# Optimization experiments

Measured on AMD Instinct MI355X. Metric: run time of the kernel, lower is better.

Reference implementation:

```python
import jax, jax.numpy as jnp
import numpy as np

B, F, V, E, D1, DD, L2 = 4096, 32, 50000, 64, 256, 16, 128


def setup_inputs() -> dict:
    key = jax.random.key(0)
    ks = jax.random.split(key, 16)
    s = 0.05  # small init scale to keep tanh unsaturated
    return {
        "sparse": jax.random.randint(ks[0], (B, F), 0, V, dtype=jnp.int32),
        "dense": jax.random.normal(ks[1], (B, DD), dtype=jnp.float32),
        "tables": jax.random.normal(ks[2], (F, V, E), dtype=jnp.float32) * s,
        "Wz": jax.random.normal(ks[3], (D1, F, E), dtype=jnp.float32) * s,
        "bz": jnp.zeros((D1,), jnp.float32),
        "Wpi": jax.random.normal(ks[4], (D1, F, F), dtype=jnp.float32) * s,
        "bpi": jnp.zeros((D1,), jnp.float32),
        "Wpo": jax.random.normal(ks[5], (D1, E, E), dtype=jnp.float32) * s,
        "bpo": jnp.zeros((D1,), jnp.float32),
        "B1": jax.random.normal(ks[6], (D1,), dtype=jnp.float32) * s,
        "W1": jax.random.normal(ks[7], (D1 + DD, D1), dtype=jnp.float32) * s,
        "b1": jnp.zeros((D1,), jnp.float32),
        "W2": jax.random.normal(ks[8], (D1, L2), dtype=jnp.float32) * s,
        "b2": jnp.zeros((L2,), jnp.float32),
        "W3": jax.random.normal(ks[9], (L2, 1), dtype=jnp.float32) * s,
        "b3": jnp.zeros((1,), jnp.float32),
    }


def reference(sparse, dense, tables, Wz, bz, Wpi, bpi, Wpo, bpo, B1,
              W1, b1, W2, b2, W3, b3):
    # Embedding lookup: per-field table gather -> [B, F, E]
    emb = tables[jnp.arange(F)[None, :], sparse]
    # Lz: Conv1d(in=F, kernel=E) over [B, F, E] == full contraction -> [B, D1]
    Lz = jnp.einsum('bfe,dfe->bd', emb, Wz) + bz
    # Inner product: [B, F, F], then Conv1d(in=F, kernel=F) full contraction
    inner = jnp.einsum('bie,bje->bij', emb, emb)
    Lp_inner = jnp.einsum('bij,dij->bd', inner, Wpi) + bpi
    # Outer product: sum_{i,j} x_i^T x_j == s^T s with s = sum_i x_i (exact rewrite)
    s = emb.sum(axis=1)                      # [B, E]
    outer = s[:, :, None] * s[:, None, :]    # [B, E, E]
    Lp_outer = jnp.einsum('bij,dij->bd', outer, Wpo) + bpo
    L1 = Lz + Lp_inner + Lp_outer + B1       # [B, D1]
    deep_x = jnp.concatenate([L1, dense], axis=1)  # [B, D1+DD]
    h = jnp.tanh(deep_x @ W1 + b1)
    h = jnp.tanh(h @ W2 + b2)
    out = (h @ W3 + b3)[:, 0]                # [B]
    return out
```

## Files before the change

### kernel.cpp

```cpp
#include <hip/hip_runtime.h>
#include <hip/hip_bf16.h>

#define B_    4096
#define F_    32
#define V_    50000
#define E_    64
#define D1_   256
#define DD_   16
#define L2N_  128
#define KX    3072
#define KTOT  7168
#define NKC   8

typedef __bf16 bf16x8 __attribute__((ext_vector_type(8)));
typedef float  f32x4  __attribute__((ext_vector_type(4)));

typedef __attribute__((address_space(1))) const void gvoid;
typedef __attribute__((address_space(3))) void svoid;

__device__ __forceinline__ ushort f2b(float f){
  __bf16 h = (__bf16)f; return __builtin_bit_cast(ushort, h);
}
__device__ __forceinline__ float b2f(ushort u){
  return __uint_as_float(((uint)u) << 16);
}
__device__ __forceinline__ float blo(uint u){ return __uint_as_float(u << 16); }
__device__ __forceinline__ float bhi(uint u){ return __uint_as_float(u & 0xffff0000u); }
__device__ __forceinline__ void gload16(const void* g, void* l){
  __builtin_amdgcn_global_load_lds((gvoid*)g, (svoid*)l, 16, 0, 0);
}

__global__ __launch_bounds__(256) void prep_gather(
    const float* __restrict__ Wz, const float* __restrict__ Wpi,
    const float* __restrict__ Wpo, const float* __restrict__ W1,
    const float* __restrict__ W2,
    const int* __restrict__ sparse, const float* __restrict__ tables,
    ushort* __restrict__ WBb, ushort* __restrict__ W1b, ushort* __restrict__ W2b,
    ushort* __restrict__ Xb, ushort* __restrict__ Sb) {
  __shared__ ushort gsh[4][32 * 72];
  int bid = blockIdx.x, t = threadIdx.x;
  if (bid < 640) {
    if (bid < 256) {
      int n = bid;
#pragma unroll
      for (int j = 0; j < 7; ++j) {
        int k4 = (j * 256 + t) * 4;
        float4 v;
        if (k4 < 2048)      v = *(const float4*)&Wz [(size_t)n * 2048 + k4];
        else if (k4 < 3072) v = *(const float4*)&Wpi[(size_t)n * 1024 + (k4 - 2048)];
        else                v = *(const float4*)&Wpo[(size_t)n * 4096 + (k4 - 3072)];
        ushort4 o = make_ushort4(f2b(v.x), f2b(v.y), f2b(v.z), f2b(v.w));
        *(ushort4*)&WBb[(size_t)n * KTOT + k4] = o;
      }
    } else if (bid < 512) {
      int n = bid - 256;
      float v0 = (t < 272) ? W1[(size_t)t * 256 + n] : 0.f;
      W1b[(size_t)n * 288 + t] = f2b(v0);
      if (t < 32) {
        int k2 = 256 + t;
        float v1 = (k2 < 272) ? W1[(size_t)k2 * 256 + n] : 0.f;
        W1b[(size_t)n * 288 + k2] = f2b(v1);
      }
    } else {
      int n = bid - 512;
      W2b[(size_t)n * 256 + t] = f2b(W2[(size_t)t * 128 + n]);
    }
    return;
  }

  int w = t >> 6, l = t & 63;
  int b = (bid - 640) * 4 + w;
  int fr = l & 15, q = l >> 4;

  int i0 = sparse[b * F_ + fr];
  int i1 = sparse[b * F_ + 16 + fr];
  const float* r0 = tables + ((size_t)fr * V_ + i0) * 64;
  const float* r1 = tables + ((size_t)(16 + fr) * V_ + i1) * 64;

  float4 v[2][2][2];
#pragma unroll
  for (int ks = 0; ks < 2; ++ks) {
    v[0][ks][0] = *(const float4*)(r0 + ks * 32 + q * 8);
    v[0][ks][1] = *(const float4*)(r0 + ks * 32 + q * 8 + 4);
    v[1][ks][0] = *(const float4*)(r1 + ks * 32 + q * 8);
    v[1][ks][1] = *(const float4*)(r1 + ks * 32 + q * 8 + 4);
  }

  bf16x8 fg[2][2];
#pragma unroll
  for (int rh = 0; rh < 2; ++rh)
#pragma unroll
    for (int ks = 0; ks < 2; ++ks) {
      bf16x8 a;
      a[0] = (__bf16)v[rh][ks][0].x; a[1] = (__bf16)v[rh][ks][0].y;
      a[2] = (__bf16)v[rh][ks][0].z; a[3] = (__bf16)v[rh][ks][0].w;
      a[4] = (__bf16)v[rh][ks][1].x; a[5] = (__bf16)v[rh][ks][1].y;
      a[6] = (__bf16)v[rh][ks][1].z; a[7] = (__bf16)v[rh][ks][1].w;
      fg[rh][ks] = a;
      *(bf16x8*)&Xb[(size_t)b * KX + (rh * 16 + fr) * 64 + ks * 32 + q * 8] = a;
    }

  float sv[2][8];
#pragma unroll
  for (int ks = 0; ks < 2; ++ks) {
    sv[ks][0] = v[0][ks][0].x + v[1][ks][0].x; sv[ks][1] = v[0][ks][0].y + v[1][ks][0].y;
    sv[ks][2] = v[0][ks][0].z + v[1][ks][0].z; sv[ks][3] = v[0][ks][0].w + v[1][ks][0].w;
    sv[ks][4] = v[0][ks][1].x + v[1][ks][1].x; sv[ks][5] = v[0][ks][1].y + v[1][ks][1].y;
    sv[ks][6] = v[0][ks][1].z + v[1][ks][1].z; sv[ks][7] = v[0][ks][1].w + v[1][ks][1].w;
  }
#pragma unroll
  for (int m = 1; m < 16; m <<= 1)
#pragma unroll
    for (int ks = 0; ks < 2; ++ks)
#pragma unroll
      for (int j = 0; j < 8; ++j)
        sv[ks][j] += __shfl_xor(sv[ks][j], m, 64);
  if (fr == 0) {
#pragma unroll
    for (int ks = 0; ks < 2; ++ks) {
      ushort4 o0 = make_ushort4(f2b(sv[ks][0]), f2b(sv[ks][1]), f2b(sv[ks][2]), f2b(sv[ks][3]));
      ushort4 o1 = make_ushort4(f2b(sv[ks][4]), f2b(sv[ks][5]), f2b(sv[ks][6]), f2b(sv[ks][7]));
      *(ushort4*)&Sb[(size_t)b * 64 + ks * 32 + q * 8]     = o0;
      *(ushort4*)&Sb[(size_t)b * 64 + ks * 32 + q * 8 + 4] = o1;
    }
  }

  f32x4 g[2][2] = {};
#pragma unroll
  for (int ks = 0; ks < 2; ++ks)
#pragma unroll
    for (int ri = 0; ri < 2; ++ri)
#pragma unroll
      for (int rj = 0; rj < 2; ++rj)
        g[ri][rj] = __builtin_amdgcn_mfma_f32_16x16x32_bf16(
            fg[ri][ks], fg[rj][ks], g[ri][rj], 0, 0, 0);

#pragma unroll
  for (int ri = 0; ri < 2; ++ri)
#pragma unroll
    for (int rj = 0; rj < 2; ++rj)
#pragma unroll
      for (int r = 0; r < 4; ++r)
        gsh[w][(ri * 16 + q * 4 + r) * 72 + rj * 16 + fr] = f2b(g[ri][rj][r]);
  {
    int rrow = l >> 1, rcol = (l & 1) * 16;
    uint4 ga = *(const uint4*)&gsh[w][rrow * 72 + rcol];
    uint4 gb = *(const uint4*)&gsh[w][rrow * 72 + rcol + 8];
    size_t dst = (size_t)b * KX + 2048 + rrow * 32 + rcol;
    *(uint4*)&Xb[dst]     = ga;
    *(uint4*)&Xb[dst + 8] = gb;
  }
}

__global__ __launch_bounds__(512, 1) void gemm_l1(
    const ushort* __restrict__ Xb, const ushort* __restrict__ WBb,
    const ushort* __restrict__ Sb, ushort* __restrict__ Lp) {
  __shared__ __align__(16) ushort As[2][128 * 64];
  __shared__ __align__(16) ushort Bs[2][256 * 64];
  __shared__ ushort Ssl[128 * 18];

  int bid = blockIdx.x;
  int kc  = bid & 7;
  int mT  = bid >> 3;
  int bRow = mT * 128;
  int kt0 = kc * 14;
  int i_start = min(max(0, kt0 - 48), 48);

  int tid = threadIdx.x, w = tid >> 6, l = tid & 63;
  int wm = (w >> 2) * 64, wn = (w & 3) * 64;
  int fr = l & 15, q = l >> 4;

#pragma unroll
  for (int r = 0; r < 2; ++r) {
    int p = r * 1024 + tid * 2;
    int row = p >> 4, col = p & 15;
    *(ushort2*)&Ssl[row * 18 + col] =
        *(const ushort2*)&Sb[(size_t)(bRow + row) * 64 + i_start + col];
  }

  uint4 sregu[4][2];
#pragma unroll
  for (int mi = 0; mi < 4; ++mi) {
    int grow = bRow + wm + mi * 16 + fr;
    sregu[mi][0] = *(const uint4*)&Sb[(size_t)grow * 64 + q * 8];
    sregu[mi][1] = *(const uint4*)&Sb[(size_t)grow * 64 + 32 + q * 8];
  }

  int r8 = l >> 3;
  int sg = ((l & 7) ^ r8) * 8;

  auto stageA = [&](int bI, int kt) {
    const ushort* src = Xb + (size_t)(bRow + w * 16 + r8) * KX + kt * 64 + sg;
#pragma unroll
    for (int c = 0; c < 2; ++c)
      gload16(src + (size_t)(c * 8) * KX, &As[bI][(w * 16 + c * 8) * 64]);
  };
  auto stageB = [&](int bI, int kt) {
    const ushort* src = WBb + (size_t)(w * 32 + r8) * KTOT + kt * 64 + sg;
#pragma unroll
    for (int c = 0; c < 4; ++c)
      gload16(src + (size_t)(c * 8) * KTOT, &Bs[bI][(w * 32 + c * 8) * 64]);
  };

  f32x4 acc[4][4] = {};
  bf16x8 af[4][2], bfr[4][2];
  int buf = 0;

  if (kt0 < 48) stageA(0, kt0);
  stageB(0, kt0);
  __syncthreads();

#pragma unroll
  for (int tl = 0; tl < 14; ++tl) {
    int kt = kt0 + tl;
    if (tl + 1 < 14) {
      if (kt + 1 < 48) stageA(buf ^ 1, kt + 1);
      stageB(buf ^ 1, kt + 1);
    }

#pragma unroll
    for (int ni = 0; ni < 4; ++ni) {
      int col = wn + ni * 16 + fr;
#pragma unroll
      for (int ks = 0; ks < 2; ++ks) {
        int slot = (ks * 4 + q) ^ (col & 7);
        bfr[ni][ks] = *(const bf16x8*)&Bs[buf][col * 64 + slot * 8];
      }
    }
    if (kt < 48) {
#pragma unroll
      for (int mi = 0; mi < 4; ++mi) {
        int row = wm + mi * 16 + fr;
#pragma unroll
        for (int ks = 0; ks < 2; ++ks) {
          int slot = (ks * 4 + q) ^ (row & 7);
          af[mi][ks] = *(const bf16x8*)&As[buf][row * 64 + slot * 8];
        }
      }
    } else {
      int iloc = kt - 48 - i_start;
#pragma unroll
      for (int mi = 0; mi < 4; ++mi) {
        float si = b2f(Ssl[(wm + mi * 16 + fr) * 18 + iloc]);
#pragma unroll
        for (int ks = 0; ks < 2; ++ks) {
          uint4 uv = sregu[mi][ks];
          bf16x8 a;
          a[0] = (__bf16)(si * blo(uv.x)); a[1] = (__bf16)(si * bhi(uv.x));
          a[2] = (__bf16)(si * blo(uv.y)); a[3] = (__bf16)(si * bhi(uv.y));
          a[4] = (__bf16)(si * blo(uv.z)); a[5] = (__bf16)(si * bhi(uv.z));
          a[6] = (__bf16)(si * blo(uv.w)); a[7] = (__bf16)(si * bhi(uv.w));
          af[mi][ks] = a;
        }
      }
    }
#pragma unroll
    for (int ks = 0; ks < 2; ++ks)
#pragma unroll
      for (int mi = 0; mi < 4; ++mi)
#pragma unroll
        for (int ni = 0; ni < 4; ++ni)
          acc[mi][ni] = __builtin_amdgcn_mfma_f32_16x16x32_bf16(
              af[mi][ks], bfr[ni][ks], acc[mi][ni], 0, 0, 0);
    __syncthreads();
    buf ^= 1;
  }

  ushort* Lpk = Lp + (size_t)kc * (B_ * D1_);
#pragma unroll
  for (int mi = 0; mi < 4; ++mi) {
    int row0 = bRow + wm + mi * 16 + q * 4;
#pragma unroll
    for (int ni = 0; ni < 4; ++ni) {
      int col = wn + ni * 16 + fr;
#pragma unroll
      for (int r = 0; r < 4; ++r)
        Lpk[(size_t)(row0 + r) * D1_ + col] = f2b(acc[mi][ni][r]);
    }
  }
}

__global__ __launch_bounds__(256) void mlp_fused(
    const ushort* __restrict__ Lp, const float* __restrict__ dense,
    const ushort* __restrict__ W1b, const ushort* __restrict__ W2b,
    const float* __restrict__ bz, const float* __restrict__ bpi,
    const float* __restrict__ bpo, const float* __restrict__ B1v,
    const float* __restrict__ b1, const float* __restrict__ b2,
    const float* __restrict__ W3, const float* __restrict__ b3,
    float* __restrict__ out) {
  __shared__ ushort hs[16 * 264];
  __shared__ ushort h2s[16 * 136];
  __shared__ float bvs[256];
  int b0 = blockIdx.x * 16;
  int tid = threadIdx.x, w = tid >> 6, l = tid & 63;
  int row = l & 15, q = l >> 4;
  int wn = w * 64;

  bvs[tid] = bz[tid] + bpi[tid] + bpo[tid] + B1v[tid];
  __syncthreads();

  f32x4 acc1[4] = {};
  for (int kt = 0; kt < 9; ++kt) {
    int k0 = kt * 32 + q * 8;
    bf16x8 afr;
    if (kt < 8) {
      size_t base = (size_t)(b0 + row) * D1_ + k0;
      float s[8] = {0.f, 0.f, 0.f, 0.f, 0.f, 0.f, 0.f, 0.f};
#pragma unroll
      for (int p = 0; p < NKC; ++p) {
        uint4 u = *(const uint4*)&Lp[(size_t)p * (B_ * D1_) + base];
        s[0] += blo(u.x); s[1] += bhi(u.x);
        s[2] += blo(u.y); s[3] += bhi(u.y);
        s[4] += blo(u.z); s[5] += bhi(u.z);
        s[6] += blo(u.w); s[7] += bhi(u.w);
      }
      float4 bv0 = *(const float4*)&bvs[k0];
      float4 bv1 = *(const float4*)&bvs[k0 + 4];
      afr[0] = (__bf16)(s[0] + bv0.x); afr[1] = (__bf16)(s[1] + bv0.y);
      afr[2] = (__bf16)(s[2] + bv0.z); afr[3] = (__bf16)(s[3] + bv0.w);
      afr[4] = (__bf16)(s[4] + bv1.x); afr[5] = (__bf16)(s[5] + bv1.y);
      afr[6] = (__bf16)(s[6] + bv1.z); afr[7] = (__bf16)(s[7] + bv1.w);
    } else if (q < 2) {
      float4 u0 = *(const float4*)&dense[(size_t)(b0 + row) * DD_ + q * 8];
      float4 u1 = *(const float4*)&dense[(size_t)(b0 + row) * DD_ + q * 8 + 4];
      afr[0] = (__bf16)u0.x; afr[1] = (__bf16)u0.y; afr[2] = (__bf16)u0.z; afr[3] = (__bf16)u0.w;
      afr[4] = (__bf16)u1.x; afr[5] = (__bf16)u1.y; afr[6] = (__bf16)u1.z; afr[7] = (__bf16)u1.w;
    } else {
      afr = (bf16x8)(__bf16)0.f;
    }
#pragma unroll
    for (int ni = 0; ni < 4; ++ni) {
      bf16x8 bfr = *(const bf16x8*)&W1b[(size_t)(wn + ni * 16 + row) * 288 + k0];
      acc1[ni] = __builtin_amdgcn_mfma_f32_16x16x32_bf16(afr, bfr, acc1[ni], 0, 0, 0);
    }
  }
#pragma unroll
  for (int ni = 0; ni < 4; ++ni) {
    int col = wn + ni * 16 + row;
    float bias = b1[col];
#pragma unroll
    for (int r = 0; r < 4; ++r)
      hs[(q * 4 + r) * 264 + col] = f2b(tanhf(acc1[ni][r] + bias));
  }
  __syncthreads();

  int wn2 = w * 32;
  f32x4 acc2[2] = {};
  for (int kt = 0; kt < 8; ++kt) {
    int k0 = kt * 32 + q * 8;
    bf16x8 afr = *(const bf16x8*)&hs[row * 264 + k0];
#pragma unroll
    for (int ni = 0; ni < 2; ++ni) {
      bf16x8 bfr = *(const bf16x8*)&W2b[(size_t)(wn2 + ni * 16 + row) * 256 + k0];
      acc2[ni] = __builtin_amdgcn_mfma_f32_16x16x32_bf16(afr, bfr, acc2[ni], 0, 0, 0);
    }
  }
#pragma unroll
  for (int ni = 0; ni < 2; ++ni) {
    int col = wn2 + ni * 16 + row;
    float bias = b2[col];
#pragma unroll
    for (int r = 0; r < 4; ++r)
      h2s[(q * 4 + r) * 136 + col] = f2b(tanhf(acc2[ni][r] + bias));
  }
  __syncthreads();

  if (w == 0) {
    int rr = l >> 2, g = l & 3;
    float sum = 0.f;
#pragma unroll
    for (int jj = 0; jj < 32; ++jj) {
      int j = g * 32 + jj;
      sum += b2f(h2s[rr * 136 + j]) * W3[j];
    }
    sum += __shfl_xor(sum, 1, 64);
    sum += __shfl_xor(sum, 2, 64);
    if (g == 0) out[b0 + rr] = sum + b3[0];
  }
}

extern "C" void kernel_launch(void* const* d_in, const int* in_sizes, int n_in,
                              void* d_out, int out_size, void* d_ws, size_t ws_size,
                              hipStream_t stream) {
  const int*   sparse = (const int*)  d_in[0];
  const float* dense  = (const float*)d_in[1];
  const float* tables = (const float*)d_in[2];
  const float* Wz     = (const float*)d_in[3];
  const float* bz     = (const float*)d_in[4];
  const float* Wpi    = (const float*)d_in[5];
  const float* bpi    = (const float*)d_in[6];
  const float* Wpo    = (const float*)d_in[7];
  const float* bpo    = (const float*)d_in[8];
  const float* B1v    = (const float*)d_in[9];
  const float* W1     = (const float*)d_in[10];
  const float* b1     = (const float*)d_in[11];
  const float* W2     = (const float*)d_in[12];
  const float* b2     = (const float*)d_in[13];
  const float* W3     = (const float*)d_in[14];
  const float* b3     = (const float*)d_in[15];
  float* out = (float*)d_out;

  char* ws = (char*)d_ws;
  ushort* Xb  = (ushort*)(ws);
  ushort* WBb = (ushort*)(ws + 25165824);
  ushort* W1b = (ushort*)(ws + 28835840);
  ushort* W2b = (ushort*)(ws + 28983296);
  ushort* Sb  = (ushort*)(ws + 29048832);
  ushort* Lp  = (ushort*)(ws + 29573120);

  prep_gather<<<dim3(1664), dim3(256), 0, stream>>>(
      Wz, Wpi, Wpo, W1, W2, sparse, tables, WBb, W1b, W2b, Xb, Sb);
  gemm_l1    <<<dim3(256),  dim3(512), 0, stream>>>(Xb, WBb, Sb, Lp);
  mlp_fused  <<<dim3(256),  dim3(256), 0, stream>>>(
      Lp, dense, W1b, W2b, bz, bpi, bpo, B1v, b1, b2, W3, b3, out);
}
```

Measured before the change: 59.77 us.

## Fuse L1 GEMM and MLP into one launch with per-tile atomic counters

Merges the split-K L1 GEMM and the MLP kernels into a single 384-block launch. The extra 128 blocks spin on a per-row-tile atomic counter until all eight K-chunks for their 128 rows are written, then run the MLP on 32 rows each. The counters are reset in the prep kernel. This removes one kernel launch boundary and lets the MLP start early for finished tiles. In exchange it relies on forward progress of the waiting blocks (deadlock risk if consumer blocks occupy CUs before producers), and the MLP blocks now use 512 threads and the large shared allocation.

Result: slower. 153.5 us (+156.9%).

```diff
diff --git a/kernel.cpp b/kernel.cpp
--- a/kernel.cpp
+++ b/kernel.cpp
@@ -36,10 +36,11 @@
     const float* __restrict__ W2,
     const int* __restrict__ sparse, const float* __restrict__ tables,
     ushort* __restrict__ WBb, ushort* __restrict__ W1b, ushort* __restrict__ W2b,
-    ushort* __restrict__ Xb, ushort* __restrict__ Sb) {
+    ushort* __restrict__ Xb, ushort* __restrict__ Sb, int* __restrict__ cnt) {
   __shared__ ushort gsh[4][32 * 72];
   int bid = blockIdx.x, t = threadIdx.x;
   if (bid < 640) {
+    if (bid == 0 && t < 32) cnt[t] = 0;
     if (bid < 256) {
       int n = bid;
 #pragma unroll
@@ -152,230 +153,258 @@
   }
 }
 
-__global__ __launch_bounds__(512, 1) void gemm_l1(
+__global__ __launch_bounds__(512, 1) void gemm_mlp(
     const ushort* __restrict__ Xb, const ushort* __restrict__ WBb,
-    const ushort* __restrict__ Sb, ushort* __restrict__ Lp) {
-  __shared__ __align__(16) ushort As[2][128 * 64];
-  __shared__ __align__(16) ushort Bs[2][256 * 64];
-  __shared__ ushort Ssl[128 * 18];
-
-  int bid = blockIdx.x;
-  int kc  = bid & 7;
-  int mT  = bid >> 3;
-  int bRow = mT * 128;
-  int kt0 = kc * 14;
-  int i_start = min(max(0, kt0 - 48), 48);
-
-  int tid = threadIdx.x, w = tid >> 6, l = tid & 63;
-  int wm = (w >> 2) * 64, wn = (w & 3) * 64;
-  int fr = l & 15, q = l >> 4;
-
-#pragma unroll
-  for (int r = 0; r < 2; ++r) {
-    int p = r * 1024 + tid * 2;
-    int row = p >> 4, col = p & 15;
-    *(ushort2*)&Ssl[row * 18 + col] =
-        *(const ushort2*)&Sb[(size_t)(bRow + row) * 64 + i_start + col];
-  }
-
-  uint4 sregu[4][2];
-#pragma unroll
-  for (int mi = 0; mi < 4; ++mi) {
-    int grow = bRow + wm + mi * 16 + fr;
-    sregu[mi][0] = *(const uint4*)&Sb[(size_t)grow * 64 + q * 8];
-    sregu[mi][1] = *(const uint4*)&Sb[(size_t)grow * 64 + 32 + q * 8];
-  }
-
-  int r8 = l >> 3;
-  int sg = ((l & 7) ^ r8) * 8;
-
-  auto stageA = [&](int bI, int kt) {
-    const ushort* src = Xb + (size_t)(bRow + w * 16 + r8) * KX + kt * 64 + sg;
-#pragma unroll
-    for (int c = 0; c < 2; ++c)
-      gload16(src + (size_t)(c * 8) * KX, &As[bI][(w * 16 + c * 8) * 64]);
-  };
-  auto stageB = [&](int bI, int kt) {
-    const ushort* src = WBb + (size_t)(w * 32 + r8) * KTOT + kt * 64 + sg;
-#pragma unroll
-    for (int c = 0; c < 4; ++c)
-      gload16(src + (size_t)(c * 8) * KTOT, &Bs[bI][(w * 32 + c * 8) * 64]);
-  };
-
-  f32x4 acc[4][4] = {};
-  bf16x8 af[4][2], bfr[4][2];
-  int buf = 0;
-
-  if (kt0 < 48) stageA(0, kt0);
-  stageB(0, kt0);
-  __syncthreads();
-
-#pragma unroll
-  for (int tl = 0; tl < 14; ++tl) {
-    int kt = kt0 + tl;
-    if (tl + 1 < 14) {
-      if (kt + 1 < 48) stageA(buf ^ 1, kt + 1);
-      stageB(buf ^ 1, kt + 1);
-    }
-
-#pragma unroll
-    for (int ni = 0; ni < 4; ++ni) {
-      int col = wn + ni * 16 + fr;
-#pragma unroll
-      for (int ks = 0; ks < 2; ++ks) {
-        int slot = (ks * 4 + q) ^ (col & 7);
-        bfr[ni][ks] = *(const bf16x8*)&Bs[buf][col * 64 + slot * 8];
-      }
-    }
-    if (kt < 48) {
-#pragma unroll
-      for (int mi = 0; mi < 4; ++mi) {
-        int row = wm + mi * 16 + fr;
-#pragma unroll
-        for (int ks = 0; ks < 2; ++ks) {
-          int slot = (ks * 4 + q) ^ (row & 7);
-          af[mi][ks] = *(const bf16x8*)&As[buf][row * 64 + slot * 8];
-        }
-      }
-    } else {
-      int iloc = kt - 48 - i_start;
-#pragma unroll
-      for (int mi = 0; mi < 4; ++mi) {
-        float si = b2f(Ssl[(wm + mi * 16 + fr) * 18 + iloc]);
-#pragma unroll
-        for (int ks = 0; ks < 2; ++ks) {
-          uint4 uv = sregu[mi][ks];
-          bf16x8 a;
-          a[0] = (__bf16)(si * blo(uv.x)); a[1] = (__bf16)(si * bhi(uv.x));
-          a[2] = (__bf16)(si * blo(uv.y)); a[3] = (__bf16)(si * bhi(uv.y));
-          a[4] = (__bf16)(si * blo(uv.z)); a[5] = (__bf16)(si * bhi(uv.z));
-          a[6] = (__bf16)(si * blo(uv.w)); a[7] = (__bf16)(si * bhi(uv.w));
-          af[mi][ks] = a;
-        }
-      }
-    }
-#pragma unroll
-    for (int ks = 0; ks < 2; ++ks)
-#pragma unroll
-      for (int mi = 0; mi < 4; ++mi)
-#pragma unroll
-        for (int ni = 0; ni < 4; ++ni)
-          acc[mi][ni] = __builtin_amdgcn_mfma_f32_16x16x32_bf16(
-              af[mi][ks], bfr[ni][ks], acc[mi][ni], 0, 0, 0);
-    __syncthreads();
-    buf ^= 1;
-  }
-
-  ushort* Lpk = Lp + (size_t)kc * (B_ * D1_);
-#pragma unroll
-  for (int mi = 0; mi < 4; ++mi) {
-    int row0 = bRow + wm + mi * 16 + q * 4;
-#pragma unroll
-    for (int ni = 0; ni < 4; ++ni) {
-      int col = wn + ni * 16 + fr;
-#pragma unroll
-      for (int r = 0; r < 4; ++r)
-        Lpk[(size_t)(row0 + r) * D1_ + col] = f2b(acc[mi][ni][r]);
-    }
-  }
-}
-
-__global__ __launch_bounds__(256) void mlp_fused(
-    const ushort* __restrict__ Lp, const float* __restrict__ dense,
+    const ushort* __restrict__ Sb, ushort* __restrict__ Lp,
+    const float* __restrict__ dense,
     const ushort* __restrict__ W1b, const ushort* __restrict__ W2b,
     const float* __restrict__ bz, const float* __restrict__ bpi,
     const float* __restrict__ bpo, const float* __restrict__ B1v,
     const float* __restrict__ b1, const float* __restrict__ b2,
     const float* __restrict__ W3, const float* __restrict__ b3,
-    float* __restrict__ out) {
-  __shared__ ushort hs[16 * 264];
-  __shared__ ushort h2s[16 * 136];
-  __shared__ float bvs[256];
-  int b0 = blockIdx.x * 16;
+    int* __restrict__ cnt, float* __restrict__ out) {
+  __shared__ __align__(16) ushort smem[51456];
+
+  int bid = blockIdx.x;
   int tid = threadIdx.x, w = tid >> 6, l = tid & 63;
-  int row = l & 15, q = l >> 4;
-  int wn = w * 64;
-
-  bvs[tid] = bz[tid] + bpi[tid] + bpo[tid] + B1v[tid];
-  __syncthreads();
-
-  f32x4 acc1[4] = {};
-  for (int kt = 0; kt < 9; ++kt) {
-    int k0 = kt * 32 + q * 8;
-    bf16x8 afr;
-    if (kt < 8) {
-      size_t base = (size_t)(b0 + row) * D1_ + k0;
-      float s[8] = {0.f, 0.f, 0.f, 0.f, 0.f, 0.f, 0.f, 0.f};
-#pragma unroll
-      for (int p = 0; p < NKC; ++p) {
-        uint4 u = *(const uint4*)&Lp[(size_t)p * (B_ * D1_) + base];
-        s[0] += blo(u.x); s[1] += bhi(u.x);
-        s[2] += blo(u.y); s[3] += bhi(u.y);
-        s[4] += blo(u.z); s[5] += bhi(u.z);
-        s[6] += blo(u.w); s[7] += bhi(u.w);
-      }
-      float4 bv0 = *(const float4*)&bvs[k0];
-      float4 bv1 = *(const float4*)&bvs[k0 + 4];
-      afr[0] = (__bf16)(s[0] + bv0.x); afr[1] = (__bf16)(s[1] + bv0.y);
-      afr[2] = (__bf16)(s[2] + bv0.z); afr[3] = (__bf16)(s[3] + bv0.w);
-      afr[4] = (__bf16)(s[4] + bv1.x); afr[5] = (__bf16)(s[5] + bv1.y);
-      afr[6] = (__bf16)(s[6] + bv1.z); afr[7] = (__bf16)(s[7] + bv1.w);
-    } else if (q < 2) {
-      float4 u0 = *(const float4*)&dense[(size_t)(b0 + row) * DD_ + q * 8];
-      float4 u1 = *(const float4*)&dense[(size_t)(b0 + row) * DD_ + q * 8 + 4];
-      afr[0] = (__bf16)u0.x; afr[1] = (__bf16)u0.y; afr[2] = (__bf16)u0.z; afr[3] = (__bf16)u0.w;
-      afr[4] = (__bf16)u1.x; afr[5] = (__bf16)u1.y; afr[6] = (__bf16)u1.z; afr[7] = (__bf16)u1.w;
-    } else {
-      afr = (bf16x8)(__bf16)0.f;
+  int fr = l & 15, q = l >> 4;
+
+  if (bid < 256) {
+    ushort* As0 = smem;
+    ushort* As1 = As0 + 128 * 64;
+    ushort* Bs0 = As1 + 128 * 64;
+    ushort* Bs1 = Bs0 + 256 * 64;
+    ushort* Ssl = Bs1 + 256 * 64;
+
+    int kc  = bid & 7;
+    int mT  = bid >> 3;
+    int bRow = mT * 128;
+    int kt0 = kc * 14;
+    int i_start = min(max(0, kt0 - 48), 48);
+
+    int wm = (w >> 2) * 64, wn = (w & 3) * 64;
+
+#pragma unroll
+    for (int r = 0; r < 2; ++r) {
+      int p = r * 1024 + tid * 2;
+      int row = p >> 4, col = p & 15;
+      *(ushort2*)&Ssl[row * 18 + col] =
+          *(const ushort2*)&Sb[(size_t)(bRow + row) * 64 + i_start + col];
+    }
+
+    uint4 sregu[4][2];
+#pragma unroll
+    for (int mi = 0; mi < 4; ++mi) {
+      int grow = bRow + wm + mi * 16 + fr;
+      sregu[mi][0] = *(const uint4*)&Sb[(size_t)grow * 64 + q * 8];
+      sregu[mi][1] = *(const uint4*)&Sb[(size_t)grow * 64 + 32 + q * 8];
+    }
+
+    int r8 = l >> 3;
+    int sg = ((l & 7) ^ r8) * 8;
+
+    auto stageA = [&](ushort* dst, int kt) {
+      const ushort* src = Xb + (size_t)(bRow + w * 16 + r8) * KX + kt * 64 + sg;
+#pragma unroll
+      for (int c = 0; c < 2; ++c)
+        gload16(src + (size_t)(c * 8) * KX, &dst[(w * 16 + c * 8) * 64]);
+    };
+    auto stageB = [&](ushort* dst, int kt) {
+      const ushort* src = WBb + (size_t)(w * 32 + r8) * KTOT + kt * 64 + sg;
+#pragma unroll
+      for (int c = 0; c < 4; ++c)
+        gload16(src + (size_t)(c * 8) * KTOT, &dst[(w * 32 + c * 8) * 64]);
+    };
+
+    f32x4 acc[4][4] = {};
+    bf16x8 af[4][2], bfr[4][2];
+
+    if (kt0 < 48) stageA(As0, kt0);
+    stageB(Bs0, kt0);
+    __syncthreads();
+
+#pragma unroll
+    for (int tl = 0; tl < 14; ++tl) {
+      int kt = kt0 + tl;
+      ushort* Ac = (tl & 1) ? As1 : As0;
+      ushort* Bc = (tl & 1) ? Bs1 : Bs0;
+      ushort* An = (tl & 1) ? As0 : As1;
+      ushort* Bn = (tl & 1) ? Bs0 : Bs1;
+      if (tl + 1 < 14) {
+        if (kt + 1 < 48) stageA(An, kt + 1);
+        stageB(Bn, kt + 1);
+      }
+
+#pragma unroll
+      for (int ni = 0; ni < 4; ++ni) {
+        int col = wn + ni * 16 + fr;
+#pragma unroll
+        for (int ks = 0; ks < 2; ++ks) {
+          int slot = (ks * 4 + q) ^ (col & 7);
+          bfr[ni][ks] = *(const bf16x8*)&Bc[col * 64 + slot * 8];
+        }
+      }
+      if (kt < 48) {
+#pragma unroll
+        for (int mi = 0; mi < 4; ++mi) {
+          int row = wm + mi * 16 + fr;
+#pragma unroll
+          for (int ks = 0; ks < 2; ++ks) {
+            int slot = (ks * 4 + q) ^ (row & 7);
+            af[mi][ks] = *(const bf16x8*)&Ac[row * 64 + slot * 8];
+          }
+        }
+      } else {
+        int iloc = kt - 48 - i_start;
+#pragma unroll
+        for (int mi = 0; mi < 4; ++mi) {
+          float si = b2f(Ssl[(wm + mi * 16 + fr) * 18 + iloc]);
+#pragma unroll
+          for (int ks = 0; ks < 2; ++ks) {
+            uint4 uv = sregu[mi][ks];
+            bf16x8 a;
+            a[0] = (__bf16)(si * blo(uv.x)); a[1] = (__bf16)(si * bhi(uv.x));
+            a[2] = (__bf16)(si * blo(uv.y)); a[3] = (__bf16)(si * bhi(uv.y));
+            a[4] = (__bf16)(si * blo(uv.z)); a[5] = (__bf16)(si * bhi(uv.z));
+            a[6] = (__bf16)(si * blo(uv.w)); a[7] = (__bf16)(si * bhi(uv.w));
+            af[mi][ks] = a;
+          }
+        }
+      }
+#pragma unroll
+      for (int ks = 0; ks < 2; ++ks)
+#pragma unroll
+        for (int mi = 0; mi < 4; ++mi)
+#pragma unroll
+          for (int ni = 0; ni < 4; ++ni)
+            acc[mi][ni] = __builtin_amdgcn_mfma_f32_16x16x32_bf16(
+                af[mi][ks], bfr[ni][ks], acc[mi][ni], 0, 0, 0);
+      __syncthreads();
+    }
+
+    ushort* Lpk = Lp + (size_t)kc * (B_ * D1_);
+#pragma unroll
+    for (int mi = 0; mi < 4; ++mi) {
+      int row0 = bRow + wm + mi * 16 + q * 4;
+#pragma unroll
+      for (int ni = 0; ni < 4; ++ni) {
+        int col = wn + ni * 16 + fr;
+#pragma unroll
+        for (int r = 0; r < 4; ++r)
+          Lpk[(size_t)(row0 + r) * D1_ + col] = f2b(acc[mi][ni][r]);
+      }
+    }
+
+    __threadfence();
+    __syncthreads();
+    if (tid == 0) atomicAdd(&cnt[mT], 1);
+    return;
+  }
+
+  {
+    int bid2 = bid - 256;
+    int b0   = bid2 * 32;
+    int mT   = bid2 >> 2;
+
+    if (tid == 0) {
+      while (__hip_atomic_load(&cnt[mT], __ATOMIC_RELAXED,
+                               __HIP_MEMORY_SCOPE_AGENT) < NKC)
+        __builtin_amdgcn_s_sleep(8);
+    }
+    __syncthreads();
+    __threadfence();
+
+    ushort* hs  = smem;
+    ushort* h2s = smem + 32 * 264;
+    float*  bvs = (float*)(smem + 32 * 264 + 32 * 136);
+
+    if (tid < 256) bvs[tid] = bz[tid] + bpi[tid] + bpo[tid] + B1v[tid];
+    __syncthreads();
+
+    int rg = w >> 2;
+    int cg = w & 3;
+    int row = fr;
+    int rr = rg * 16;
+
+    int wn1 = cg * 64;
+    f32x4 acc1[4] = {};
+    for (int kt = 0; kt < 9; ++kt) {
+      int k0 = kt * 32 + q * 8;
+      bf16x8 afr;
+      if (kt < 8) {
+        size_t base = (size_t)(b0 + rr + row) * D1_ + k0;
+        float s[8] = {0.f, 0.f, 0.f, 0.f, 0.f, 0.f, 0.f, 0.f};
+#pragma unroll
+        for (int p = 0; p < NKC; ++p) {
+          uint4 u = *(const uint4*)&Lp[(size_t)p * (B_ * D1_) + base];
+          s[0] += blo(u.x); s[1] += bhi(u.x);
+          s[2] += blo(u.y); s[3] += bhi(u.y);
+          s[4] += blo(u.z); s[5] += bhi(u.z);
+          s[6] += blo(u.w); s[7] += bhi(u.w);
+        }
+        float4 bv0 = *(const float4*)&bvs[k0];
+        float4 bv1 = *(const float4*)&bvs[k0 + 4];
+        afr[0] = (__bf16)(s[0] + bv0.x); afr[1] = (__bf16)(s[1] + bv0.y);
+        afr[2] = (__bf16)(s[2] + bv0.z); afr[3] = (__bf16)(s[3] + bv0.w);
+        afr[4] = (__bf16)(s[4] + bv1.x); afr[5] = (__bf16)(s[5] + bv1.y);
+        afr[6] = (__bf16)(s[6] + bv1.z); afr[7] = (__bf16)(s[7] + bv1.w);
+      } else if (q < 2) {
+        float4 u0 = *(const float4*)&dense[(size_t)(b0 + rr + row) * DD_ + q * 8];
+        float4 u1 = *(const float4*)&dense[(size_t)(b0 + rr + row) * DD_ + q * 8 + 4];
+        afr[0] = (__bf16)u0.x; afr[1] = (__bf16)u0.y; afr[2] = (__bf16)u0.z; afr[3] = (__bf16)u0.w;
+        afr[4] = (__bf16)u1.x; afr[5] = (__bf16)u1.y; afr[6] = (__bf16)u1.z; afr[7] = (__bf16)u1.w;
+      } else {
+        afr = (bf16x8)(__bf16)0.f;
+      }
+#pragma unroll
+      for (int ni = 0; ni < 4; ++ni) {
+        bf16x8 bfr = *(const bf16x8*)&W1b[(size_t)(wn1 + ni * 16 + row) * 288 + k0];
+        acc1[ni] = __builtin_amdgcn_mfma_f32_16x16x32_bf16(afr, bfr, acc1[ni], 0, 0, 0);
+      }
     }
 #pragma unroll
     for (int ni = 0; ni < 4; ++ni) {
-      bf16x8 bfr = *(const bf16x8*)&W1b[(size_t)(wn + ni * 16 + row) * 288 + k0];
-      acc1[ni] = __builtin_amdgcn_mfma_f32_16x16x32_bf16(afr, bfr, acc1[ni], 0, 0, 0);
-    }
-  }
-#pragma unroll
-  for (int ni = 0; ni < 4; ++ni) {
-    int col = wn + ni * 16 + row;
-    float bias = b1[col];
-#pragma unroll
-    for (int r = 0; r < 4; ++r)
-      hs[(q * 4 + r) * 264 + col] = f2b(tanhf(acc1[ni][r] + bias));
-  }
-  __syncthreads();
-
-  int wn2 = w * 32;
-  f32x4 acc2[2] = {};
-  for (int kt = 0; kt < 8; ++kt) {
-    int k0 = kt * 32 + q * 8;
-    bf16x8 afr = *(const bf16x8*)&hs[row * 264 + k0];
+      int col = wn1 + ni * 16 + row;
+      float bias = b1[col];
+#pragma unroll
+      for (int r = 0; r < 4; ++r)
+        hs[(rr + q * 4 + r) * 264 + col] = f2b(tanhf(acc1[ni][r] + bias));
+    }
+    __syncthreads();
+
+    int wn2 = cg * 32;
+    f32x4 acc2[2] = {};
+    for (int kt = 0; kt < 8; ++kt) {
+      int k0 = kt * 32 + q * 8;
+      bf16x8 afr = *(const bf16x8*)&hs[(rr + row) * 264 + k0];
+#pragma unroll
+      for (int ni = 0; ni < 2; ++ni) {
+        bf16x8 bfr = *(const bf16x8*)&W2b[(size_t)(wn2 + ni * 16 + row) * 256 + k0];
+        acc2[ni] = __builtin_amdgcn_mfma_f32_16x16x32_bf16(afr, bfr, acc2[ni], 0, 0, 0);
+      }
+    }
 #pragma unroll
     for (int ni = 0; ni < 2; ++ni) {
-      bf16x8 bfr = *(const bf16x8*)&W2b[(size_t)(wn2 + ni * 16 + row) * 256 + k0];
-      acc2[ni] = __builtin_amdgcn_mfma_f32_16x16x32_bf16(afr, bfr, acc2[ni], 0, 0, 0);
-    }
-  }
-#pragma unroll
-  for (int ni = 0; ni < 2; ++ni) {
-    int col = wn2 + ni * 16 + row;
-    float bias = b2[col];
-#pragma unroll
-    for (int r = 0; r < 4; ++r)
-      h2s[(q * 4 + r) * 136 + col] = f2b(tanhf(acc2[ni][r] + bias));
-  }
-  __syncthreads();
-
-  if (w == 0) {
-    int rr = l >> 2, g = l & 3;
-    float sum = 0.f;
-#pragma unroll
-    for (int jj = 0; jj < 32; ++jj) {
-      int j = g * 32 + jj;
-      sum += b2f(h2s[rr * 136 + j]) * W3[j];
-    }
-    sum += __shfl_xor(sum, 1, 64);
-    sum += __shfl_xor(sum, 2, 64);
-    if (g == 0) out[b0 + rr] = sum + b3[0];
+      int col = wn2 + ni * 16 + row;
+      float bias = b2[col];
+#pragma unroll
+      for (int r = 0; r < 4; ++r)
+        h2s[(rr + q * 4 + r) * 136 + col] = f2b(tanhf(acc2[ni][r] + bias));
+    }
+    __syncthreads();
+
+    if (w < 2) {
+      int rl = w * 16 + (l >> 2), g = l & 3;
+      float sum = 0.f;
+#pragma unroll
+      for (int jj = 0; jj < 32; ++jj) {
+        int j = g * 32 + jj;
+        sum += b2f(h2s[rl * 136 + j]) * W3[j];
+      }
+      sum += __shfl_xor(sum, 1, 64);
+      sum += __shfl_xor(sum, 2, 64);
+      if (g == 0) out[b0 + rl] = sum + b3[0];
+    }
   }
 }
 
@@ -407,10 +436,11 @@
   ushort* W2b = (ushort*)(ws + 28983296);
   ushort* Sb  = (ushort*)(ws + 29048832);
   ushort* Lp  = (ushort*)(ws + 29573120);
+  int*    cnt = (int*)   (ws + 46350336);
 
   prep_gather<<<dim3(1664), dim3(256), 0, stream>>>(
-      Wz, Wpi, Wpo, W1, W2, sparse, tables, WBb, W1b, W2b, Xb, Sb);
-  gemm_l1    <<<dim3(256),  dim3(512), 0, stream>>>(Xb, WBb, Sb, Lp);
-  mlp_fused  <<<dim3(256),  dim3(256), 0, stream>>>(
-      Lp, dense, W1b, W2b, bz, bpi, bpo, B1v, b1, b2, W3, b3, out);
-}
+      Wz, Wpi, Wpo, W1, W2, sparse, tables, WBb, W1b, W2b, Xb, Sb, cnt);
+  gemm_mlp   <<<dim3(384),  dim3(512), 0, stream>>>(
+      Xb, WBb, Sb, Lp, dense, W1b, W2b, bz, bpi, bpo, B1v,
+      b1, b2, W3, b3, cnt, out);
+}
```
